# Kernel tuning notes

Measured on AMD Instinct MI355X. Metric: run time of the kernel, lower is better.

Reference implementation:

```python
import jax, jax.numpy as jnp
import numpy as np

N_NODES = 20000
N_EDGES = 320000
F_IN = 64      # num_node_features
C = 64         # out_features (per-head channels, concat=False)
H = 4          # n_heads
L = 3          # n_layers (stackable since F_IN == C)
N_RES = 2
N_PAIRS = 8192
EDGE_DIM = 9
HID = 64 * C   # ResNetGated hidden dim = 64 * out_features
N_EXPERTS = 8


def setup_inputs() -> dict:
    key = jax.random.key(0)
    ks = jax.random.split(key, 24)
    s = 0.05
    f32 = jnp.float32
    inp = {}
    inp["x"] = jax.random.normal(ks[0], (N_NODES, F_IN), f32)
    inp["edge_index"] = jax.random.randint(ks[1], (2, N_EDGES), 0, N_NODES)
    inp["edge_attr"] = jax.random.normal(ks[2], (N_EDGES, EDGE_DIM), f32)
    inp["edge_cross"] = jax.random.randint(ks[3], (N_PAIRS, 2), 0, N_NODES)
    inp["types"] = jax.random.randint(ks[4], (N_PAIRS,), 0, N_EXPERTS)
    # GATv2 encoder params, stacked over L layers (layer 0 in-dim == C)
    inp["gat_Wl"] = jax.random.normal(ks[5], (L, F_IN, H * C), f32) * s
    inp["gat_bl"] = jnp.full((L, H * C), 0.01, f32)
    inp["gat_Wr"] = jax.random.normal(ks[6], (L, F_IN, H * C), f32) * s
    inp["gat_br"] = jnp.full((L, H * C), 0.01, f32)
    inp["gat_We"] = jax.random.normal(ks[7], (L, EDGE_DIM, H * C), f32) * s  # lin_edge, no bias
    inp["gat_att"] = jax.random.normal(ks[8], (L, H, C), f32) * s
    inp["gat_bias"] = jnp.zeros((L, C), f32)
    inp["gat_gates"] = jax.random.normal(ks[9], (L,), f32) * 0.5
    # 8 type-routed experts: ResNetGated(2C -> 64C -> 2C) x N_RES, then Linear(2C, 1)
    inp["res_W1"] = jax.random.normal(ks[10], (N_EXPERTS, N_RES, 2 * C, HID), f32) * s
    inp["res_b1"] = jnp.full((N_EXPERTS, N_RES, HID), 0.01, f32)
    inp["res_W2"] = jax.random.normal(ks[11], (N_EXPERTS, N_RES, HID, 2 * C), f32) * s
    inp["res_b2"] = jnp.full((N_EXPERTS, N_RES, 2 * C), 0.01, f32)
    inp["res_gates"] = jax.random.normal(ks[12], (N_EXPERTS, N_RES), f32) * 0.5
    inp["head_W"] = jax.random.normal(ks[13], (N_EXPERTS, 2 * C, 1), f32) * s
    inp["head_b"] = jnp.full((N_EXPERTS, 1), 0.01, f32)
    return inp


def _gat_layer(h, src, tgt, ea, Wl, bl, Wr, br, We, att, bias):
    # GATv2Conv with edge features, concat=False (mean over heads)
    n = h.shape[0]
    nh, c = att.shape
    xl = (h @ Wl + bl).reshape(n, nh, c)   # source transform (x_j)
    xr = (h @ Wr + br).reshape(n, nh, c)   # target transform (x_i)
    e = (ea @ We).reshape(-1, nh, c)
    m = jax.nn.leaky_relu(xl[src] + xr[tgt] + e, 0.2)       # [E,H,C]
    logits = jnp.einsum('ehc,hc->eh', m, att)               # [E,H]
    mx = jax.ops.segment_max(logits, tgt, num_segments=n)
    a = jnp.exp(logits - mx[tgt])
    den = jax.ops.segment_sum(a, tgt, num_segments=n)
    alpha = a / den[tgt]                                     # segment softmax over in-edges
    out = jax.ops.segment_sum(xl[src] * alpha[:, :, None], tgt, num_segments=n)
    return out.mean(axis=1) + bias


def reference(x, edge_index, edge_attr, edge_cross, types,
              gat_Wl, gat_bl, gat_Wr, gat_br, gat_We, gat_att, gat_bias, gat_gates,
              res_W1, res_b1, res_W2, res_b2, res_gates, head_W, head_b):
    src, tgt = edge_index[0], edge_index[1]
    g = jax.nn.sigmoid(gat_gates)
    h = _gat_layer(x, src, tgt, edge_attr, gat_Wl[0], gat_bl[0], gat_Wr[0], gat_br[0],
                   gat_We[0], gat_att[0], gat_bias[0])
    for i in range(1, gat_Wl.shape[0]):
        h = jax.nn.leaky_relu(h, 0.01)
        hi = _gat_layer(h, src, tgt, edge_attr, gat_Wl[i], gat_bl[i], gat_Wr[i], gat_br[i],
                        gat_We[i], gat_att[i], gat_bias[i])
        h = g[i - 1] * hi + (1 - g[i - 1]) * h
    # pair gather + feature interleave: x[edge_cross].transpose(1,2).reshape(P, 2C)
    pair = h[edge_cross]                               # [P,2,C]
    p = pair.shape[0]
    z0 = jnp.swapaxes(pair, 1, 2).reshape(p, -1)        # [P,2C]
    outs = []
    for e in range(res_W1.shape[0]):
        z = z0
        ge = jax.nn.sigmoid(res_gates[e])
        for r in range(res_W1.shape[1]):
            z = jax.nn.relu(z)
            y = jax.nn.relu(z @ res_W1[e, r] + res_b1[e, r]) @ res_W2[e, r] + res_b2[e, r]
            z = ge[r] * y + (1 - ge[r]) * z
        outs.append(z @ head_W[e] + head_b[e])          # [P,1]
    all_out = jnp.stack(outs)                           # [8,P,1]
    per_row = all_out[types, jnp.arange(p)]             # [P,1] per-row expert output
    order = jnp.argsort(types, stable=True)             # concat groups type 0..7, stable in-group
    return per_row[order]
```

## Files before the change

kernel.cpp:

```cpp
#include <hip/hip_runtime.h>

#define NN 20000
#define NE 320000
#define NL 3
#define NP 8192
#define EDIM 9
#define TROWS 32
#define MAXT 272
#define CAPR (MAXT*TROWS)

typedef _Float16 f16x8 __attribute__((ext_vector_type(8)));
typedef float f32x4 __attribute__((ext_vector_type(4)));

#define GLL16(g,l) __builtin_amdgcn_global_load_lds((const __attribute__((address_space(1))) unsigned int*)(g), (__attribute__((address_space(3))) unsigned int*)(l), 16, 0, 0)

__device__ __forceinline__ float sigm(float x){ return 1.f/(1.f+__expf(-x)); }

__device__ __forceinline__ float dpp_sum64(float x){
  x += __int_as_float(__builtin_amdgcn_update_dpp(0, __float_as_int(x), 0x111, 0xf, 0xf, true));
  x += __int_as_float(__builtin_amdgcn_update_dpp(0, __float_as_int(x), 0x112, 0xf, 0xf, true));
  x += __int_as_float(__builtin_amdgcn_update_dpp(0, __float_as_int(x), 0x114, 0xf, 0xf, true));
  x += __int_as_float(__builtin_amdgcn_update_dpp(0, __float_as_int(x), 0x118, 0xf, 0xf, true));
  x += __int_as_float(__builtin_amdgcn_update_dpp(0, __float_as_int(x), 0x142, 0xf, 0xf, true));
  x += __int_as_float(__builtin_amdgcn_update_dpp(0, __float_as_int(x), 0x143, 0xf, 0xf, true));
  return __uint_as_float(__builtin_amdgcn_readlane(__float_as_uint(x), 63));
}

__global__ void k_fill_i(int* __restrict__ p, int n, int v){ int i=blockIdx.x*blockDim.x+threadIdx.x; if(i<n)p[i]=v; }

__global__ void k_deg(const int* __restrict__ ei, int* __restrict__ deg){
  int e=blockIdx.x*blockDim.x+threadIdx.x; if(e<NE) atomicAdd(&deg[ei[NE+e]],1);
}

__global__ __launch_bounds__(1024) void k_scan(const int* __restrict__ deg, int* __restrict__ row_ptr, int* __restrict__ cursor){
  __shared__ int sh[1024];
  __shared__ int carry;
  int tid=threadIdx.x;
  if(tid==0) carry=0;
  __syncthreads();
  for(int base=0;base<NN;base+=1024){
    int i=base+tid;
    int v=(i<NN)?deg[i]:0;
    sh[tid]=v; __syncthreads();
    for(int o=1;o<1024;o<<=1){
      int t=(tid>=o)?sh[tid-o]:0; __syncthreads();
      sh[tid]+=t; __syncthreads();
    }
    int incl=sh[tid];
    int c=carry;
    if(i<NN){ row_ptr[i+1]=c+incl; cursor[i]=c+incl-v; }
    if(i==0) row_ptr[0]=0;
    __syncthreads();
    if(tid==1023) carry=c+incl;
    __syncthreads();
  }
}

__global__ void k_fill_csr2(const int* __restrict__ ei, const float* __restrict__ ea,
    int* __restrict__ cursor, int* __restrict__ csr_src, float* __restrict__ eas){
  int e=blockIdx.x*blockDim.x+threadIdx.x;
  if(e<NE){
    int t=ei[NE+e]; int pos=atomicAdd(&cursor[t],1);
    csr_src[pos]=ei[e];
    const float* s=ea+(size_t)e*9;
    float* d=eas+(size_t)pos*12;
    #pragma unroll
    for(int k=0;k<9;++k) d[k]=s[k];
    d[9]=0.f; d[10]=0.f; d[11]=0.f;
  }
}

__global__ __launch_bounds__(256) void k_sort(const int* __restrict__ types, int* __restrict__ meta,
    int* __restrict__ slotp, int* __restrict__ islot){
  __shared__ int cnt[256][8];
  __shared__ int tot[8];
  __shared__ int base_s[8], pad_s[8];
  int tid=threadIdx.x;
  int lc[8]={0,0,0,0,0,0,0,0};
  int tl[32];
  for(int i=0;i<32;++i){ int ty=types[tid*32+i]; tl[i]=ty; lc[ty]++; }
  #pragma unroll
  for(int t=0;t<8;++t) cnt[tid][t]=lc[t];
  __syncthreads();
  if(tid<8){
    int run=0;
    for(int j=0;j<256;++j){ int v=cnt[j][tid]; cnt[j][tid]=run; run+=v; }
    tot[tid]=run;
  }
  __syncthreads();
  if(tid==0){
    int b=0, pb=0, nt=0;
    for(int t=0;t<8;++t){
      base_s[t]=b; pad_s[t]=pb;
      meta[t]=tot[t]; meta[8+t]=b; meta[16+t]=pb;
      int ntt=(tot[t]+31)>>5;
      for(int j=0;j<ntt;++j){ meta[32+nt]=t; meta[32+MAXT+nt]=pb+j*32; nt++; }
      b+=tot[t]; pb+=ntt*32;
    }
    meta[24]=nt; meta[25]=pb;
  }
  __syncthreads();
  if(tid<8){
    int t=tid; int ntt=(tot[t]+31)>>5;
    for(int sr=tot[t]; sr<ntt*32; ++sr) islot[pad_s[t]+sr]=-1;
  }
  int run[8];
  #pragma unroll
  for(int t=0;t<8;++t) run[t]=cnt[tid][t];
  for(int i=0;i<32;++i){
    int p=tid*32+i; int t=tl[i]; int r=run[t]++;
    int pos=base_s[t]+r, slot=pad_s[t]+r;
    slotp[p]=slot; islot[slot]=pos;
  }
}

__global__ __launch_bounds__(256) void k_nodexf(const float* __restrict__ hin,
    const float* __restrict__ Wl, const float* __restrict__ bl,
    const float* __restrict__ Wr, const float* __restrict__ br,
    float* __restrict__ xl, float* __restrict__ xr, int lk){
  __shared__ float hs[64][66];
  __shared__ float ws[64][66];
  int n0=blockIdx.x*64, tid=threadIdx.x;
  for(int idx=tid; idx<64*64; idx+=256){
    int r=idx>>6,k=idx&63; int n=n0+r;
    float v=(n<NN)?hin[(size_t)n*64+k]:0.f;
    if(lk) v=v>0.f?v:0.01f*v;
    hs[r][k]=v;
  }
  int ty=tid>>4, tx=tid&15;
  for(int ch=0; ch<8; ++ch){
    const float* W=(ch<4)?Wl:Wr;
    const float* bb=(ch<4)?bl:br;
    float* outp=(ch<4)?xl:xr;
    int c0=(ch&3)*64;
    __syncthreads();
    for(int idx=tid; idx<64*64; idx+=256){ int k=idx>>6,j=idx&63; ws[k][j]=W[(size_t)k*256+c0+j]; }
    __syncthreads();
    float acc[4][4]={};
    #pragma unroll 4
    for(int k=0;k<64;++k){
      float a0=hs[4*ty+0][k],a1=hs[4*ty+1][k],a2=hs[4*ty+2][k],a3=hs[4*ty+3][k];
      float b0=ws[k][4*tx+0],b1v=ws[k][4*tx+1],b2v=ws[k][4*tx+2],b3v=ws[k][4*tx+3];
      acc[0][0]+=a0*b0; acc[0][1]+=a0*b1v; acc[0][2]+=a0*b2v; acc[0][3]+=a0*b3v;
      acc[1][0]+=a1*b0; acc[1][1]+=a1*b1v; acc[1][2]+=a1*b2v; acc[1][3]+=a1*b3v;
      acc[2][0]+=a2*b0; acc[2][1]+=a2*b1v; acc[2][2]+=a2*b2v; acc[2][3]+=a2*b3v;
      acc[3][0]+=a3*b0; acc[3][1]+=a3*b1v; acc[3][2]+=a3*b2v; acc[3][3]+=a3*b3v;
    }
    #pragma unroll
    for(int i=0;i<4;++i){
      int n=n0+4*ty+i;
      if(n<NN){
        #pragma unroll
        for(int j=0;j<4;++j){ int c=c0+4*tx+j; outp[(size_t)n*256+c]=acc[i][j]+bb[c]; }
      }
    }
  }
}

__global__ __launch_bounds__(256) void k_agg2(const float* __restrict__ xl, const float* __restrict__ xr,
    const float* __restrict__ eas, const int* __restrict__ csr_src, const int* __restrict__ row_ptr,
    const float* __restrict__ WeL, const float* __restrict__ attL,
    const float* __restrict__ biasL, const float* __restrict__ gates, int layer,
    const float* __restrict__ hprev, float* __restrict__ hout){
  __shared__ float red[4][64];
  int n=blockIdx.x, tid=threadIdx.x;
  float w0=WeL[tid],      w1=WeL[256+tid],  w2=WeL[512+tid],  w3=WeL[768+tid],  w4=WeL[1024+tid];
  float w5=WeL[1280+tid], w6=WeL[1536+tid], w7=WeL[1792+tid], w8=WeL[2048+tid];
  float att_t=attL[tid];
  float xr_t=xr[(size_t)n*256+tid];
  int s=row_ptr[n], t=row_ptr[n+1];
  float den=0.f, acc=0.f;

  auto body=[&](float xlv, int j){
    const float4* ep=(const float4*)(eas+(size_t)j*12);
    float4 e0=ep[0], e1=ep[1];
    float e8=eas[(size_t)j*12+8];
    float ev=e0.x*w0+e0.y*w1+e0.z*w2+e0.w*w3+e1.x*w4+e1.y*w5+e1.z*w6+e1.w*w7+e8*w8;
    float m=xlv+xr_t+ev;
    m=m>0.f?m:0.2f*m;
    float pt=dpp_sum64(m*att_t);
    float a=__expf(pt);
    den+=a; acc+=a*xlv;
  };

  float x0=0.f,x1=0.f,x2=0.f,x3=0.f;
  if(s+0<t) x0=xl[(size_t)csr_src[s+0]*256+tid];
  if(s+1<t) x1=xl[(size_t)csr_src[s+1]*256+tid];
  if(s+2<t) x2=xl[(size_t)csr_src[s+2]*256+tid];
  if(s+3<t) x3=xl[(size_t)csr_src[s+3]*256+tid];
  int j=s;
  while(j+7<t){
    float y0=xl[(size_t)csr_src[j+4]*256+tid];
    float y1=xl[(size_t)csr_src[j+5]*256+tid];
    float y2=xl[(size_t)csr_src[j+6]*256+tid];
    float y3=xl[(size_t)csr_src[j+7]*256+tid];
    body(x0,j); body(x1,j+1); body(x2,j+2); body(x3,j+3);
    x0=y0; x1=y1; x2=y2; x3=y3;
    j+=4;
  }
  if(j<t){ body(x0,j); ++j; }
  if(j<t){ body(x1,j); ++j; }
  if(j<t){ body(x2,j); ++j; }
  if(j<t){ body(x3,j); ++j; }
  while(j<t){ body(xl[(size_t)csr_src[j]*256+tid], j); ++j; }

  float rdn=den>0.f?1.f/den:0.f;
  int h=tid>>6, cc=tid&63;
  red[h][cc]=acc*rdn;
  __syncthreads();
  if(tid<64){
    float mean=(red[0][tid]+red[1][tid]+red[2][tid]+red[3][tid])*0.25f + biasL[tid];
    float o;
    if(layer==0) o=mean;
    else{
      float hp=hprev[(size_t)n*64+tid];
      hp=hp>0.f?hp:0.01f*hp;
      float g=sigm(gates[layer-1]);
      o=g*mean+(1.f-g)*hp;
    }
    hout[(size_t)n*64+tid]=o;
  }
}

__global__ void k_buildz(const float* __restrict__ hfin, const int* __restrict__ ecross,
    const int* __restrict__ slotp, float* __restrict__ z){
  int g=blockIdx.x*blockDim.x+threadIdx.x;
  if(g>=NP*64) return;
  int p=g>>6, c=g&63;
  int a=ecross[2*p], b=ecross[2*p+1];
  int slot=slotp[p];
  float2 v; v.x=hfin[(size_t)a*64+c]; v.y=hfin[(size_t)b*64+c];
  ((float2*)(z+(size_t)slot*128))[c]=v;
}

__global__ __launch_bounds__(256) void k_prepw1(const float* __restrict__ src, _Float16* __restrict__ dst){
  __shared__ float lds[128][33];
  int bid=blockIdx.x, er=bid>>7, ch=bid&127;
  const float* s=src+(size_t)er*128*4096 + ch*32;
  int tid=threadIdx.x;
  for(int idx=tid; idx<128*32; idx+=256){ int k=idx>>5, jl=idx&31; lds[k][jl]=s[(size_t)k*4096+jl]; }
  __syncthreads();
  _Float16* d=dst+(size_t)bid*4096;
  for(int g=tid; g<512; g+=256){
    int jl=g>>4, k8=g&15;
    f16x8 v;
    #pragma unroll
    for(int t=0;t<8;++t) v[t]=(_Float16)lds[k8*8+t][jl];
    int elem=(jl*128+k8*8)^((jl&7)<<3);
    *(f16x8*)(&d[elem])=v;
  }
}

__global__ __launch_bounds__(256) void k_prepw2(const float* __restrict__ src, _Float16* __restrict__ dst){
  __shared__ float lds[32][130];
  int bid=blockIdx.x, er=bid>>7, ch=bid&127;
  const float* s=src+(size_t)er*4096*128 + (size_t)ch*32*128;
  int tid=threadIdx.x;
  for(int idx=tid; idx<32*128; idx+=256){ int j=idx>>7, n=idx&127; lds[j][n]=s[(size_t)j*128+n]; }
  __syncthreads();
  _Float16* d=dst+(size_t)bid*4096;
  for(int g=tid; g<512; g+=256){
    int n=g>>2, j8=g&3;
    f16x8 v;
    #pragma unroll
    for(int t=0;t<8;++t) v[t]=(_Float16)lds[j8*8+t][n];
    int elem=(n*32+j8*8)^((n&7)<<3);
    *(f16x8*)(&d[elem])=v;
  }
}

__global__ __launch_bounds__(256) void k_resmfma(const float* __restrict__ zin,
    const _Float16* __restrict__ w1t, const _Float16* __restrict__ w2t,
    const float* __restrict__ b1all, const int* __restrict__ meta,
    float* __restrict__ ypart, int rb)
{
  __shared__ _Float16 zh[32*128];
  __shared__ _Float16 wb[2][8192];
  __shared__ _Float16 ts[32*32];
  __shared__ float b1s[1024];
  int bidl=blockIdx.x;
  int bid=(bidl&7)*132+(bidl>>3);
  int v=bid>>2, hq=bid&3;
  int nt=meta[24];
  if(v>=nt) return;
  int e=meta[32+v], row0=meta[32+MAXT+v];
  int er=e*2+rb;
  const _Float16* w1b=w1t+(size_t)er*524288 + (size_t)hq*32*4096;
  const _Float16* w2b=w2t+(size_t)er*524288 + (size_t)hq*32*4096;
  const float* b1g=b1all+(size_t)er*4096 + hq*1024;
  int tid=threadIdx.x, l=tid&63, w=tid>>6;
  int lm=l&15, lq=l>>4;
  int s16=(w&1)*16, jh=w>>1;
  int arow=s16+lm;

  for(int g=tid; g<512; g+=256){
    int row=g>>4, slot=g&15;
    const float* src=zin+(size_t)(row0+row)*128+slot*8;
    float4 v0=*(const float4*)src;
    float4 v1=*(const float4*)(src+4);
    f16x8 hv;
    hv[0]=(_Float16)fmaxf(v0.x,0.f); hv[1]=(_Float16)fmaxf(v0.y,0.f);
    hv[2]=(_Float16)fmaxf(v0.z,0.f); hv[3]=(_Float16)fmaxf(v0.w,0.f);
    hv[4]=(_Float16)fmaxf(v1.x,0.f); hv[5]=(_Float16)fmaxf(v1.y,0.f);
    hv[6]=(_Float16)fmaxf(v1.z,0.f); hv[7]=(_Float16)fmaxf(v1.w,0.f);
    *(f16x8*)(&zh[(row*128+slot*8)^((row&7)<<3)])=hv;
  }
  for(int g=tid; g<1024; g+=256) b1s[g]=b1g[g];

  #pragma unroll
  for(int s=0;s<2;++s){
    int so=(w*2+s)*512;
    GLL16(w1b+so+l*8, &wb[0][so]);
    GLL16(w2b+so+l*8, &wb[0][4096+so]);
  }
  asm volatile("s_waitcnt lgkmcnt(0)" ::: "memory");
  __builtin_amdgcn_sched_barrier(0);
  __builtin_amdgcn_s_barrier();

  f32x4 yacc[4];
  #pragma unroll
  for(int i=0;i<4;++i){ yacc[i][0]=0.f; yacc[i][1]=0.f; yacc[i][2]=0.f; yacc[i][3]=0.f; }

  for(int cc=0; cc<32; ++cc){
    int buf=cc&1;
    if(cc<31){
      const _Float16* g1=w1b+(size_t)(cc+1)*4096;
      const _Float16* g2=w2b+(size_t)(cc+1)*4096;
      int nb=buf^1;
      #pragma unroll
      for(int s=0;s<2;++s){
        int so=(w*2+s)*512;
        GLL16(g1+so+l*8, &wb[nb][so]);
        GLL16(g2+so+l*8, &wb[nb][4096+so]);
      }
      asm volatile("s_waitcnt vmcnt(4)" ::: "memory");
    }else{
      asm volatile("s_waitcnt vmcnt(0)" ::: "memory");
    }
    __builtin_amdgcn_sched_barrier(0);
    __builtin_amdgcn_s_barrier();

    f32x4 tacc={0.f,0.f,0.f,0.f};
    int j=jh*16+lm;
    #pragma unroll
    for(int ks=0;ks<4;++ks){
      f16x8 a=*(const f16x8*)(&zh[(arow*128+ks*32+lq*8)^((arow&7)<<3)]);
      f16x8 b=*(const f16x8*)(&wb[buf][(j*128+ks*32+lq*8)^((j&7)<<3)]);
      tacc=__builtin_amdgcn_mfma_f32_16x16x32_f16(a,b,tacc,0,0,0);
    }
    float b1v=b1s[cc*32+j];
    #pragma unroll
    for(int r=0;r<4;++r){
      int trow=s16+lq*4+r;
      ts[(trow*32+j)^((trow&7)<<3)]=(_Float16)fmaxf(tacc[r]+b1v,0.f);
    }
    asm volatile("s_waitcnt lgkmcnt(0)" ::: "memory");
    __builtin_amdgcn_sched_barrier(0);
    __builtin_amdgcn_s_barrier();

    f16x8 a2=*(const f16x8*)(&ts[(arow*32+lq*8)^((arow&7)<<3)]);
    #pragma unroll
    for(int nf=0;nf<4;++nf){
      int n=jh*64+nf*16+lm;
      f16x8 b=*(const f16x8*)(&wb[buf][4096+((n*32+lq*8)^((n&7)<<3))]);
      yacc[nf]=__builtin_amdgcn_mfma_f32_16x16x32_f16(a2,b,yacc[nf],0,0,0);
    }
    __builtin_amdgcn_s_barrier();
  }

  float* yp=ypart+(size_t)hq*CAPR*128;
  #pragma unroll
  for(int nf=0;nf<4;++nf){
    int col=jh*64+nf*16+lm;
    #pragma unroll
    for(int r=0;r<4;++r)
      yp[(size_t)(row0+s16+lq*4+r)*128+col]=yacc[nf][r];
  }
}

__global__ __launch_bounds__(256) void k_comb(const float* __restrict__ zin, const float* __restrict__ ypart,
    const float* __restrict__ b2all, const float* __restrict__ gates, const int* __restrict__ meta,
    int rb, float* __restrict__ zout,
    const float* __restrict__ hWg, const float* __restrict__ hbg, const int* __restrict__ islot,
    float* __restrict__ out)
{
  int v=blockIdx.x;
  if(v>=meta[24]) return;
  int e=meta[32+v], row0=meta[32+MAXT+v];
  int er=e*2+rb;
  float ge=sigm(gates[er]);
  const float* b2=b2all+(size_t)er*128;
  int tid=threadIdx.x;
  const size_t HS=(size_t)CAPR*128;
  if(rb==0){
    for(int idx=tid; idx<32*128; idx+=256){
      int r=idx>>7, c=idx&127;
      size_t o=(size_t)(row0+r)*128+c;
      float y=ypart[o]+ypart[HS+o]+ypart[2*HS+o]+ypart[3*HS+o];
      float zr=fmaxf(zin[o],0.f);
      zout[o]=ge*(y+b2[c])+(1.f-ge)*zr;
    }
  }else{
    int r=tid>>3, cs=tid&7;
    float acc=0.f;
    size_t ro=(size_t)(row0+r)*128;
    #pragma unroll
    for(int q=0;q<16;++q){
      int c=cs*16+q;
      size_t o=ro+c;
      float y=ypart[o]+ypart[HS+o]+ypart[2*HS+o]+ypart[3*HS+o];
      float zr=fmaxf(zin[o],0.f);
      float zf=ge*(y+b2[c])+(1.f-ge)*zr;
      acc+=zf*hWg[e*128+c];
    }
    acc+=__shfl_xor(acc,1); acc+=__shfl_xor(acc,2); acc+=__shfl_xor(acc,4);
    if(cs==0){
      int pos=islot[row0+r];
      if(pos>=0) out[pos]=acc+hbg[e];
    }
  }
}

extern "C" void kernel_launch(void* const* d_in, const int* in_sizes, int n_in,
                              void* d_out, int out_size, void* d_ws, size_t ws_size,
                              hipStream_t stream){
  const float* x     =(const float*)d_in[0];
  const int*   ei    =(const int*)  d_in[1];
  const float* ea    =(const float*)d_in[2];
  const int*   ecross=(const int*)  d_in[3];
  const int*   types =(const int*)  d_in[4];
  const float* gWl   =(const float*)d_in[5];
  const float* gbl   =(const float*)d_in[6];
  const float* gWr   =(const float*)d_in[7];
  const float* gbr   =(const float*)d_in[8];
  const float* gWe   =(const float*)d_in[9];
  const float* gatt  =(const float*)d_in[10];
  const float* gbias =(const float*)d_in[11];
  const float* ggate =(const float*)d_in[12];
  const float* rW1   =(const float*)d_in[13];
  const float* rb1   =(const float*)d_in[14];
  const float* rW2   =(const float*)d_in[15];
  const float* rb2   =(const float*)d_in[16];
  const float* rg    =(const float*)d_in[17];
  const float* hW    =(const float*)d_in[18];
  const float* hb    =(const float*)d_in[19];
  float* out=(float*)d_out;

  char* base=(char*)d_ws;
  size_t off=0;
  auto alloc=[&](size_t bytes)->char*{
    char* p=base+off;
    off=(off+bytes+511)&~((size_t)511);
    return p;
  };
  float* hA     =(float*)alloc((size_t)NN*64*4);
  float* hB     =(float*)alloc((size_t)NN*64*4);
  int*   deg    =(int*)  alloc((size_t)NN*4);
  int*   row_ptr=(int*)  alloc((size_t)(NN+1)*4);
  int*   cursor =(int*)  alloc((size_t)NN*4);
  int*   csr_src=(int*)  alloc((size_t)(NE+16)*4);
  int*   meta   =(int*)  alloc(1024*4);
  int*   slotp  =(int*)  alloc((size_t)NP*4);
  int*   islot  =(int*)  alloc((size_t)CAPR*4);
  float* zA     =(float*)alloc((size_t)CAPR*128*4);
  size_t uoff=off;
  float* xl =(float*)(base+uoff);
  float* xr =(float*)(base+uoff+(size_t)NN*256*4);
  float* eas=(float*)(base+uoff+(size_t)NN*256*4*2);
  _Float16* w1t=(_Float16*)(base+uoff);
  _Float16* w2t=(_Float16*)(base+uoff+(size_t)16*524288*2);
  float* ypart =(float*)(base+uoff+(size_t)16*524288*2*2);
  size_t gat_bytes=(size_t)NN*256*4*2 + (size_t)(NE*12+16)*4;
  size_t exp_bytes=(size_t)16*524288*2*2 + (size_t)4*CAPR*128*4;
  size_t need=uoff+(gat_bytes>exp_bytes?gat_bytes:exp_bytes);
  if(ws_size<need) return;
  float* zB=hB;

  k_fill_i<<<(NN+255)/256,256,0,stream>>>(deg,NN,0);
  k_deg<<<(NE+255)/256,256,0,stream>>>(ei,deg);
  k_scan<<<1,1024,0,stream>>>(deg,row_ptr,cursor);
  k_fill_csr2<<<(NE+255)/256,256,0,stream>>>(ei,ea,cursor,csr_src,eas);
  k_sort<<<1,256,0,stream>>>(types,meta,slotp,islot);

  const float* hcur=x;
  float* hnext=hA;
  for(int L=0;L<NL;++L){
    k_nodexf<<<(NN+63)/64,256,0,stream>>>(hcur, gWl+(size_t)L*64*256, gbl+(size_t)L*256,
                                          gWr+(size_t)L*64*256, gbr+(size_t)L*256, xl, xr, L>0?1:0);
    k_agg2<<<NN,256,0,stream>>>(xl,xr,eas,csr_src,row_ptr, gWe+(size_t)L*EDIM*256,
                                gatt+(size_t)L*256, gbias+(size_t)L*64, ggate, L, hcur, hnext);
    hcur=hnext;
    hnext=(hcur==hA)?hB:hA;
  }

  k_buildz<<<NP*64/256,256,0,stream>>>(hcur,ecross,slotp,zA);

  k_prepw1<<<2048,256,0,stream>>>(rW1,w1t);
  k_prepw2<<<2048,256,0,stream>>>(rW2,w2t);

  k_resmfma<<<1056,256,0,stream>>>(zA,w1t,w2t,rb1,meta,ypart,0);
  k_comb<<<MAXT,256,0,stream>>>(zA,ypart,rb2,rg,meta,0,zB,hW,hb,islot,out);
  k_resmfma<<<1056,256,0,stream>>>(zB,w1t,w2t,rb1,meta,ypart,1);
  k_comb<<<MAXT,256,0,stream>>>(zB,ypart,rb2,rg,meta,1,zA,hW,hb,islot,out);

  (void)in_sizes; (void)n_in; (void)out_size;
}
```

Before: 669.2 us.

## Split node transform across column chunks and vectorize LDS and global accesses

The node-feature transform kernel now launches one block per (64-node tile, 64-column chunk) pair instead of looping over 8 chunks inside each block. This raises the grid from about 313 to about 2500 blocks, which should fill the GPU better. The input tile is stored transposed in LDS so each thread reads its A and B fragments with float4 loads, and outputs and bias use float4 accesses. The cost is that the input tile is reloaded 8 times, once per chunk, though that data is small and likely cache-resident.

```diff
diff --git a/kernel.cpp b/kernel.cpp
--- a/kernel.cpp
+++ b/kernel.cpp
@@ -118,41 +118,53 @@
     const float* __restrict__ Wl, const float* __restrict__ bl,
     const float* __restrict__ Wr, const float* __restrict__ br,
     float* __restrict__ xl, float* __restrict__ xr, int lk){
-  __shared__ float hs[64][66];
-  __shared__ float ws[64][66];
-  int n0=blockIdx.x*64, tid=threadIdx.x;
-  for(int idx=tid; idx<64*64; idx+=256){
-    int r=idx>>6,k=idx&63; int n=n0+r;
-    float v=(n<NN)?hin[(size_t)n*64+k]:0.f;
-    if(lk) v=v>0.f?v:0.01f*v;
-    hs[r][k]=v;
-  }
+  __shared__ float hsT[64][68];
+  __shared__ float ws[64][68];
+  int bid=blockIdx.x;
+  int n0=(bid>>3)*64, ch=bid&7;
+  const float* W=(ch<4)?Wl:Wr;
+  const float* bb=(ch<4)?bl:br;
+  float* outp=(ch<4)?xl:xr;
+  int c0=(ch&3)*64;
+  int tid=threadIdx.x;
+
+  for(int idx=tid; idx<64*16; idx+=256){
+    int r=idx&63, kq=idx>>6;
+    int n=n0+r;
+    float4 v=make_float4(0.f,0.f,0.f,0.f);
+    if(n<NN) v=*(const float4*)&hin[(size_t)n*64+kq*4];
+    if(lk){
+      v.x=v.x>0.f?v.x:0.01f*v.x; v.y=v.y>0.f?v.y:0.01f*v.y;
+      v.z=v.z>0.f?v.z:0.01f*v.z; v.w=v.w>0.f?v.w:0.01f*v.w;
+    }
+    hsT[kq*4+0][r]=v.x; hsT[kq*4+1][r]=v.y; hsT[kq*4+2][r]=v.z; hsT[kq*4+3][r]=v.w;
+  }
+  for(int idx=tid; idx<64*16; idx+=256){
+    int k=idx>>4, j4=idx&15;
+    *(float4*)&ws[k][j4*4]=*(const float4*)&W[(size_t)k*256+c0+j4*4];
+  }
+  __syncthreads();
+
   int ty=tid>>4, tx=tid&15;
-  for(int ch=0; ch<8; ++ch){
-    const float* W=(ch<4)?Wl:Wr;
-    const float* bb=(ch<4)?bl:br;
-    float* outp=(ch<4)?xl:xr;
-    int c0=(ch&3)*64;
-    __syncthreads();
-    for(int idx=tid; idx<64*64; idx+=256){ int k=idx>>6,j=idx&63; ws[k][j]=W[(size_t)k*256+c0+j]; }
-    __syncthreads();
-    float acc[4][4]={};
-    #pragma unroll 4
-    for(int k=0;k<64;++k){
-      float a0=hs[4*ty+0][k],a1=hs[4*ty+1][k],a2=hs[4*ty+2][k],a3=hs[4*ty+3][k];
-      float b0=ws[k][4*tx+0],b1v=ws[k][4*tx+1],b2v=ws[k][4*tx+2],b3v=ws[k][4*tx+3];
-      acc[0][0]+=a0*b0; acc[0][1]+=a0*b1v; acc[0][2]+=a0*b2v; acc[0][3]+=a0*b3v;
-      acc[1][0]+=a1*b0; acc[1][1]+=a1*b1v; acc[1][2]+=a1*b2v; acc[1][3]+=a1*b3v;
-      acc[2][0]+=a2*b0; acc[2][1]+=a2*b1v; acc[2][2]+=a2*b2v; acc[2][3]+=a2*b3v;
-      acc[3][0]+=a3*b0; acc[3][1]+=a3*b1v; acc[3][2]+=a3*b2v; acc[3][3]+=a3*b3v;
-    }
+  float acc[4][4]={};
+  #pragma unroll 4
+  for(int k=0;k<64;++k){
+    float4 a=*(const float4*)&hsT[k][4*ty];
+    float4 b=*(const float4*)&ws[k][4*tx];
+    float aa[4]={a.x,a.y,a.z,a.w}, bbv[4]={b.x,b.y,b.z,b.w};
     #pragma unroll
     for(int i=0;i<4;++i){
-      int n=n0+4*ty+i;
-      if(n<NN){
-        #pragma unroll
-        for(int j=0;j<4;++j){ int c=c0+4*tx+j; outp[(size_t)n*256+c]=acc[i][j]+bb[c]; }
-      }
+      #pragma unroll
+      for(int j=0;j<4;++j) acc[i][j]=fmaf(aa[i],bbv[j],acc[i][j]);
+    }
+  }
+  float4 bias4=*(const float4*)&bb[c0+4*tx];
+  #pragma unroll
+  for(int i=0;i<4;++i){
+    int n=n0+4*ty+i;
+    if(n<NN){
+      float4 o=make_float4(acc[i][0]+bias4.x, acc[i][1]+bias4.y, acc[i][2]+bias4.z, acc[i][3]+bias4.w);
+      *(float4*)&outp[(size_t)n*256+c0+4*tx]=o;
     }
   }
 }
@@ -485,8 +497,8 @@
   const float* hcur=x;
   float* hnext=hA;
   for(int L=0;L<NL;++L){
-    k_nodexf<<<(NN+63)/64,256,0,stream>>>(hcur, gWl+(size_t)L*64*256, gbl+(size_t)L*256,
-                                          gWr+(size_t)L*64*256, gbr+(size_t)L*256, xl, xr, L>0?1:0);
+    k_nodexf<<<((NN+63)/64)*8,256,0,stream>>>(hcur, gWl+(size_t)L*64*256, gbl+(size_t)L*256,
+                                              gWr+(size_t)L*64*256, gbr+(size_t)L*256, xl, xr, L>0?1:0);
     k_agg2<<<NN,256,0,stream>>>(xl,xr,eas,csr_src,row_ptr, gWe+(size_t)L*EDIM*256,
                                 gatt+(size_t)L*256, gbias+(size_t)L*64, ggate, L, hcur, hnext);
     hcur=hnext;
```

Result: faster. 582.0 us (-13.0%).
